# Kernel tuning notes

Hardware: AMD Instinct MI355X
Metric: run time of the kernel (lower is better)

The kernel has to match this reference:

```python
import jax, jax.numpy as jnp
import numpy as np

T, CH, D, H, W, K = 2, 8, 4, 128, 128, 2048


def setup_inputs() -> dict:
    key = jax.random.key(0)
    k1, k2, k3, k4, k5 = jax.random.split(key, 5)
    image_real = jax.random.normal(k1, (T, D, H, W), dtype=jnp.float32)
    image_imag = jax.random.normal(k2, (T, D, H, W), dtype=jnp.float32)
    csm_real = jax.random.normal(k3, (T, CH, D, H, W), dtype=jnp.float32)
    csm_imag = jax.random.normal(k4, (T, CH, D, H, W), dtype=jnp.float32)
    # non-uniform k-space trajectory in radians/voxel, [-pi, pi)
    traj = jax.random.uniform(k5, (T, 2, K), dtype=jnp.float32,
                              minval=-np.pi, maxval=np.pi)
    return {"image_real": image_real, "image_imag": image_imag,
            "csm_real": csm_real, "csm_imag": csm_imag, "traj": traj}


def reference(image_real, image_imag, csm_real, csm_imag, traj):
    # Coil-sensitivity encode: t d h w, t ch d h w -> t ch d h w (broadcast mul)
    image = (image_real + 1j * image_imag).astype(jnp.complex64)
    csm = (csm_real + 1j * csm_imag).astype(jnp.complex64)
    multi = image[:, None] * csm                       # [t, ch, d, h, w]
    t, ch, d, h, w = multi.shape
    k = traj.shape[-1]
    # Type-2 NUFFT over (h, w): exact nonuniform DFT with centered pixel grid
    ys = (jnp.arange(h) - h // 2).astype(jnp.float32)  # [h]
    xs = (jnp.arange(w) - w // 2).astype(jnp.float32)  # [w]
    # phase[t, k, h, w] = ky*y + kx*x
    phase = (traj[:, 0, :, None, None] * ys[None, None, :, None]
             + traj[:, 1, :, None, None] * xs[None, None, None, :])
    E = jnp.exp(-1j * phase).astype(jnp.complex64).reshape(t, k, h * w)
    img_flat = multi.reshape(t, ch * d, h * w)         # [t, ch*d, h*w]
    ksp = jnp.einsum('tnp,tkp->tnk', img_flat, E)      # [t, ch*d, k]
    return ksp.reshape(t, ch, d, k)
```

## Files before the change

### kernel.cpp

```cpp
#include <hip/hip_runtime.h>
#include <math.h>

typedef __attribute__((ext_vector_type(8))) short bf16x8;
typedef __attribute__((ext_vector_type(4))) float f32x4;

#define NK   2048
#define KT   16
#define NTHR 256

#define MULTI_ELEMS (1 << 20)
#define PART_OFF    (4u << 20)

__device__ __forceinline__ unsigned short f2bf(float f) {
    union { float f; unsigned u; } v; v.f = f;
    const unsigned r = (v.u + 0x7fffu + ((v.u >> 16) & 1u)) >> 16;
    return (unsigned short)r;
}

__global__ __launch_bounds__(256)
void make_multi_bf16(const float* __restrict__ imr, const float* __restrict__ imi,
                     const float* __restrict__ csr, const float* __restrict__ csi,
                     unsigned short* __restrict__ mRb, unsigned short* __restrict__ mIb)
{
    const int gid = blockIdx.x * 256 + threadIdx.x;
    const int p   = gid * 4;
    const int x   = p & 127;
    const int y   = (p >> 7) & 127;
    const int n   = (p >> 14) & 31;
    const int t   = p >> 19;
    const int d   = n & 3;
    const int ch  = n >> 2;
    const int io  = ((t * 4 + d) * 128 + y) * 128 + x;
    const int co  = (((t * 8 + ch) * 4 + d) * 128 + y) * 128 + x;

    const float4 ar = *(const float4*)(imr + io);
    const float4 ai = *(const float4*)(imi + io);
    const float4 br = *(const float4*)(csr + co);
    const float4 bi = *(const float4*)(csi + co);

    ushort4 sr, si;
    sr.x = f2bf(ar.x*br.x - ai.x*bi.x);  si.x = f2bf(ar.x*bi.x + ai.x*br.x);
    sr.y = f2bf(ar.y*br.y - ai.y*bi.y);  si.y = f2bf(ar.y*bi.y + ai.y*br.y);
    sr.z = f2bf(ar.z*br.z - ai.z*bi.z);  si.z = f2bf(ar.z*bi.z + ai.z*br.z);
    sr.w = f2bf(ar.w*br.w - ai.w*bi.w);  si.w = f2bf(ar.w*bi.w + ai.w*br.w);
    *(ushort4*)(mRb + p) = sr;
    *(ushort4*)(mIb + p) = si;
}

__global__ __launch_bounds__(NTHR, 4)
void nufft_mfma11(const float* __restrict__ traj,
                  const unsigned short* __restrict__ mRb,
                  const unsigned short* __restrict__ mIb,
                  float* __restrict__ part)
{
    __shared__ __align__(16) unsigned char sm[16384 + 2 * 64 * 136 * 2];
    float2 (*eyT)[16] = reinterpret_cast<float2 (*)[16]>(sm);
    float2 (*exT)[16] = reinterpret_cast<float2 (*)[16]>(sm + 16384);
    unsigned short (*aLds)[64][136] =
        reinterpret_cast<unsigned short (*)[64][136]>(sm + 16384);
    float (*red)[1024] = reinterpret_cast<float (*)[1024]>(sm + 16384);

    const int b   = blockIdx.x;
    const int xcd = b & 7;
    const int t   = xcd >> 2;
    const int idx = (xcd & 3) * 128 + (b >> 3);
    const int kt  = idx >> 2;
    const int yq  = idx & 3;
    const int k0  = kt * KT;
    const int tid = threadIdx.x;

    for (int i = tid; i < 2 * 128 * KT; i += NTHR) {
        const int ax  = i >> 11;
        const int rem = i & 2047;
        const int c   = rem >> 4;
        const int kli = rem & 15;
        const float kv = traj[(t * 2 + ax) * NK + k0 + kli];
        float s, co;
        sincosf(-kv * (float)(c - 64), &s, &co);
        if (ax == 0) eyT[c][kli] = make_float2(co, s);
        else         exT[c][kli] = make_float2(co, s);
    }
    __syncthreads();

    const int wv = tid >> 6;
    const int l  = tid & 63;
    const int kl = l & 15;
    const int g  = l >> 4;
    const int xw = wv * 32 + g * 8;

    bf16x8 bEr, bEiN, bEi;
#pragma unroll
    for (int j = 0; j < 8; ++j) {
        const float2 ex = exT[xw + j][kl];
        bEr[j]  = (short)f2bf(ex.x);
        bEiN[j] = (short)f2bf(-ex.y);
        bEi[j]  = (short)(bEiN[j] ^ (short)0x8000);
    }
    __syncthreads();

    f32x4 cR0 = {0.f,0.f,0.f,0.f}, cI0 = {0.f,0.f,0.f,0.f};
    f32x4 cR1 = {0.f,0.f,0.f,0.f}, cI1 = {0.f,0.f,0.f,0.f};

    for (int pp = 0; pp < 16; ++pp) {
        const int y0 = yq * 32 + pp * 2;

#pragma unroll
        for (int q = 0; q < 4; ++q) {
            const int s  = (q * 256 + tid) * 8;
            const int nr = s >> 7;
            const int x  = s & 127;
            const int n  = nr & 31;
            const int yy = nr >> 5;
            const size_t go = (((size_t)(t * 32 + n)) << 14) + (y0 + yy) * 128 + x;
            *(bf16x8*)&aLds[0][nr][x] = *(const bf16x8*)(mRb + go);
            *(bf16x8*)&aLds[1][nr][x] = *(const bf16x8*)(mIb + go);
        }
        __syncthreads();

        {
            const bf16x8 aR0 = *(const bf16x8*)&aLds[0][kl][xw];
            const bf16x8 aI0 = *(const bf16x8*)&aLds[1][kl][xw];
            const bf16x8 aR1 = *(const bf16x8*)&aLds[0][kl + 16][xw];
            const bf16x8 aI1 = *(const bf16x8*)&aLds[1][kl + 16][xw];

            f32x4 rR0 = {0.f,0.f,0.f,0.f}, rI0 = {0.f,0.f,0.f,0.f};
            f32x4 rR1 = {0.f,0.f,0.f,0.f}, rI1 = {0.f,0.f,0.f,0.f};

            rR0 = __builtin_amdgcn_mfma_f32_16x16x32_bf16(aR0, bEr,  rR0, 0, 0, 0);
            rR0 = __builtin_amdgcn_mfma_f32_16x16x32_bf16(aI0, bEiN, rR0, 0, 0, 0);
            rI0 = __builtin_amdgcn_mfma_f32_16x16x32_bf16(aR0, bEi,  rI0, 0, 0, 0);
            rI0 = __builtin_amdgcn_mfma_f32_16x16x32_bf16(aI0, bEr,  rI0, 0, 0, 0);
            rR1 = __builtin_amdgcn_mfma_f32_16x16x32_bf16(aR1, bEr,  rR1, 0, 0, 0);
            rR1 = __builtin_amdgcn_mfma_f32_16x16x32_bf16(aI1, bEiN, rR1, 0, 0, 0);
            rI1 = __builtin_amdgcn_mfma_f32_16x16x32_bf16(aR1, bEi,  rI1, 0, 0, 0);
            rI1 = __builtin_amdgcn_mfma_f32_16x16x32_bf16(aI1, bEr,  rI1, 0, 0, 0);

            const float2 e = eyT[y0][kl];
#pragma unroll
            for (int r = 0; r < 4; ++r) {
                cR0[r] += e.x * rR0[r] - e.y * rI0[r];
                cI0[r] += e.x * rI0[r] + e.y * rR0[r];
                cR1[r] += e.x * rR1[r] - e.y * rI1[r];
                cI1[r] += e.x * rI1[r] + e.y * rR1[r];
            }
        }

        {
            const bf16x8 aR0 = *(const bf16x8*)&aLds[0][32 + kl][xw];
            const bf16x8 aI0 = *(const bf16x8*)&aLds[1][32 + kl][xw];
            const bf16x8 aR1 = *(const bf16x8*)&aLds[0][32 + kl + 16][xw];
            const bf16x8 aI1 = *(const bf16x8*)&aLds[1][32 + kl + 16][xw];

            f32x4 rR0 = {0.f,0.f,0.f,0.f}, rI0 = {0.f,0.f,0.f,0.f};
            f32x4 rR1 = {0.f,0.f,0.f,0.f}, rI1 = {0.f,0.f,0.f,0.f};

            rR0 = __builtin_amdgcn_mfma_f32_16x16x32_bf16(aR0, bEr,  rR0, 0, 0, 0);
            rR0 = __builtin_amdgcn_mfma_f32_16x16x32_bf16(aI0, bEiN, rR0, 0, 0, 0);
            rI0 = __builtin_amdgcn_mfma_f32_16x16x32_bf16(aR0, bEi,  rI0, 0, 0, 0);
            rI0 = __builtin_amdgcn_mfma_f32_16x16x32_bf16(aI0, bEr,  rI0, 0, 0, 0);
            rR1 = __builtin_amdgcn_mfma_f32_16x16x32_bf16(aR1, bEr,  rR1, 0, 0, 0);
            rR1 = __builtin_amdgcn_mfma_f32_16x16x32_bf16(aI1, bEiN, rR1, 0, 0, 0);
            rI1 = __builtin_amdgcn_mfma_f32_16x16x32_bf16(aR1, bEi,  rI1, 0, 0, 0);
            rI1 = __builtin_amdgcn_mfma_f32_16x16x32_bf16(aI1, bEr,  rI1, 0, 0, 0);

            const float2 e = eyT[y0 + 1][kl];
#pragma unroll
            for (int r = 0; r < 4; ++r) {
                cR0[r] += e.x * rR0[r] - e.y * rI0[r];
                cI0[r] += e.x * rI0[r] + e.y * rR0[r];
                cR1[r] += e.x * rR1[r] - e.y * rI1[r];
                cI1[r] += e.x * rI1[r] + e.y * rR1[r];
            }
        }
        __syncthreads();
    }

    const int slot = wv & 1;
    if (wv < 2) {
#pragma unroll
        for (int r = 0; r < 4; ++r) {
            const int nn  = g * 4 + r;
            const int i00 = (nn * 16 + kl) * 2;
            const int i10 = ((nn + 16) * 16 + kl) * 2;
            red[slot][i00]     = cR0[r];
            red[slot][i00 + 1] = cI0[r];
            red[slot][i10]     = cR1[r];
            red[slot][i10 + 1] = cI1[r];
        }
    }
    __syncthreads();
    if (wv >= 2) {
#pragma unroll
        for (int r = 0; r < 4; ++r) {
            const int nn  = g * 4 + r;
            const int i00 = (nn * 16 + kl) * 2;
            const int i10 = ((nn + 16) * 16 + kl) * 2;
            red[slot][i00]     += cR0[r];
            red[slot][i00 + 1] += cI0[r];
            red[slot][i10]     += cR1[r];
            red[slot][i10 + 1] += cI1[r];
        }
    }
    __syncthreads();

    {
        const int bp = ((t * 128 + kt) * 4 + yq) * 1024;
        for (int f = tid; f < 1024; f += NTHR)
            part[bp + f] = red[0][f] + red[1][f];
    }
}

__global__ __launch_bounds__(256)
void reduce_out(const float* __restrict__ part, float* __restrict__ out)
{
    const int gidx = blockIdx.x * 256 + threadIdx.x;
    const int t  = gidx >> 16;
    const int r1 = gidx & 65535;
    const int kt = r1 >> 9;
    const int r2 = r1 & 511;
    const int n  = r2 >> 4;
    const int kl = r2 & 15;

    const int base = ((t * 128 + kt) * 4) * 1024;
    const int fr   = (n * 16 + kl) * 2;
    float re = 0.f, im = 0.f;
#pragma unroll
    for (int yqi = 0; yqi < 4; ++yqi) {
        re += part[base + yqi * 1024 + fr];
        im += part[base + yqi * 1024 + fr + 1];
    }

    const int oi = (t * 32 + n) * 2048 + kt * KT + kl;
    out[oi]           = re;
    out[131072 + oi]  = im;
}

extern "C" void kernel_launch(void* const* d_in, const int* in_sizes, int n_in,
                              void* d_out, int out_size, void* d_ws, size_t ws_size,
                              hipStream_t stream) {
    const float* imr  = (const float*)d_in[0];
    const float* imi  = (const float*)d_in[1];
    const float* csr  = (const float*)d_in[2];
    const float* csi  = (const float*)d_in[3];
    const float* traj = (const float*)d_in[4];
    float* out = (float*)d_out;

    unsigned short* mRb = (unsigned short*)d_ws;
    unsigned short* mIb = mRb + MULTI_ELEMS;
    float* part = (float*)((char*)d_ws + PART_OFF);

    make_multi_bf16<<<dim3(1024), dim3(256), 0, stream>>>(imr, imi, csr, csi, mRb, mIb);
    nufft_mfma11<<<dim3(1024), dim3(NTHR), 0, stream>>>(traj, mRb, mIb, part);
    reduce_out<<<dim3(512), dim3(256), 0, stream>>>(part, out);
}
```

Measured before the change: 60.36 us.

## Process two 16-wide k-tiles per block to reuse staged image tiles

Each block now covers 32 k-samples instead of 16, computing two sets of MFMA products from the same LDS-staged image rows, and the grid is halved to 512 blocks. This halves global/LDS loads of the bf16 coil image per unit of work and halves the per-block sincos table setup relative to output. In exchange it doubles accumulator register use, lowers the occupancy hint to 2 blocks per SIMD set, and leaves fewer blocks to fill the GPU.

```diff
diff --git a/kernel.cpp b/kernel.cpp
--- a/kernel.cpp
+++ b/kernel.cpp
@@ -5,7 +5,6 @@
 typedef __attribute__((ext_vector_type(4))) float f32x4;
 
 #define NK   2048
-#define KT   16
 #define NTHR 256
 
 #define MULTI_ELEMS (1 << 20)
@@ -47,33 +46,33 @@
     *(ushort4*)(mIb + p) = si;
 }
 
-__global__ __launch_bounds__(NTHR, 4)
-void nufft_mfma11(const float* __restrict__ traj,
+__global__ __launch_bounds__(NTHR, 2)
+void nufft_mfma12(const float* __restrict__ traj,
                   const unsigned short* __restrict__ mRb,
                   const unsigned short* __restrict__ mIb,
                   float* __restrict__ part)
 {
-    __shared__ __align__(16) unsigned char sm[16384 + 2 * 64 * 136 * 2];
-    float2 (*eyT)[16] = reinterpret_cast<float2 (*)[16]>(sm);
-    float2 (*exT)[16] = reinterpret_cast<float2 (*)[16]>(sm + 16384);
+    __shared__ __align__(16) unsigned char sm[32768 + 2 * 64 * 136 * 2];
+    float2 (*eyT)[32] = reinterpret_cast<float2 (*)[32]>(sm);
+    float2 (*exT)[32] = reinterpret_cast<float2 (*)[32]>(sm + 32768);
     unsigned short (*aLds)[64][136] =
-        reinterpret_cast<unsigned short (*)[64][136]>(sm + 16384);
-    float (*red)[1024] = reinterpret_cast<float (*)[1024]>(sm + 16384);
+        reinterpret_cast<unsigned short (*)[64][136]>(sm + 32768);
+    float (*red)[2048] = reinterpret_cast<float (*)[2048]>(sm + 32768);
 
     const int b   = blockIdx.x;
     const int xcd = b & 7;
     const int t   = xcd >> 2;
-    const int idx = (xcd & 3) * 128 + (b >> 3);
-    const int kt  = idx >> 2;
+    const int idx = (xcd & 3) * 64 + (b >> 3);
+    const int ktp = idx >> 2;
     const int yq  = idx & 3;
-    const int k0  = kt * KT;
+    const int k0  = ktp * 32;
     const int tid = threadIdx.x;
 
-    for (int i = tid; i < 2 * 128 * KT; i += NTHR) {
-        const int ax  = i >> 11;
-        const int rem = i & 2047;
-        const int c   = rem >> 4;
-        const int kli = rem & 15;
+    for (int i = tid; i < 2 * 128 * 32; i += NTHR) {
+        const int ax  = i >> 12;
+        const int rem = i & 4095;
+        const int c   = rem >> 5;
+        const int kli = rem & 31;
         const float kv = traj[(t * 2 + ax) * NK + k0 + kli];
         float s, co;
         sincosf(-kv * (float)(c - 64), &s, &co);
@@ -88,18 +87,24 @@
     const int g  = l >> 4;
     const int xw = wv * 32 + g * 8;
 
-    bf16x8 bEr, bEiN, bEi;
+    bf16x8 bEr_a, bEiN_a, bEi_a, bEr_b, bEiN_b, bEi_b;
 #pragma unroll
     for (int j = 0; j < 8; ++j) {
-        const float2 ex = exT[xw + j][kl];
-        bEr[j]  = (short)f2bf(ex.x);
-        bEiN[j] = (short)f2bf(-ex.y);
-        bEi[j]  = (short)(bEiN[j] ^ (short)0x8000);
+        const float2 exa = exT[xw + j][kl];
+        bEr_a[j]  = (short)f2bf(exa.x);
+        bEiN_a[j] = (short)f2bf(-exa.y);
+        bEi_a[j]  = (short)(bEiN_a[j] ^ (short)0x8000);
+        const float2 exb = exT[xw + j][16 + kl];
+        bEr_b[j]  = (short)f2bf(exb.x);
+        bEiN_b[j] = (short)f2bf(-exb.y);
+        bEi_b[j]  = (short)(bEiN_b[j] ^ (short)0x8000);
     }
     __syncthreads();
 
-    f32x4 cR0 = {0.f,0.f,0.f,0.f}, cI0 = {0.f,0.f,0.f,0.f};
-    f32x4 cR1 = {0.f,0.f,0.f,0.f}, cI1 = {0.f,0.f,0.f,0.f};
+    f32x4 cR0a = {0.f,0.f,0.f,0.f}, cI0a = {0.f,0.f,0.f,0.f};
+    f32x4 cR1a = {0.f,0.f,0.f,0.f}, cI1a = {0.f,0.f,0.f,0.f};
+    f32x4 cR0b = {0.f,0.f,0.f,0.f}, cI0b = {0.f,0.f,0.f,0.f};
+    f32x4 cR1b = {0.f,0.f,0.f,0.f}, cI1b = {0.f,0.f,0.f,0.f};
 
     for (int pp = 0; pp < 16; ++pp) {
         const int y0 = yq * 32 + pp * 2;
@@ -125,23 +130,44 @@
 
             f32x4 rR0 = {0.f,0.f,0.f,0.f}, rI0 = {0.f,0.f,0.f,0.f};
             f32x4 rR1 = {0.f,0.f,0.f,0.f}, rI1 = {0.f,0.f,0.f,0.f};
-
-            rR0 = __builtin_amdgcn_mfma_f32_16x16x32_bf16(aR0, bEr,  rR0, 0, 0, 0);
-            rR0 = __builtin_amdgcn_mfma_f32_16x16x32_bf16(aI0, bEiN, rR0, 0, 0, 0);
-            rI0 = __builtin_amdgcn_mfma_f32_16x16x32_bf16(aR0, bEi,  rI0, 0, 0, 0);
-            rI0 = __builtin_amdgcn_mfma_f32_16x16x32_bf16(aI0, bEr,  rI0, 0, 0, 0);
-            rR1 = __builtin_amdgcn_mfma_f32_16x16x32_bf16(aR1, bEr,  rR1, 0, 0, 0);
-            rR1 = __builtin_amdgcn_mfma_f32_16x16x32_bf16(aI1, bEiN, rR1, 0, 0, 0);
-            rI1 = __builtin_amdgcn_mfma_f32_16x16x32_bf16(aR1, bEi,  rI1, 0, 0, 0);
-            rI1 = __builtin_amdgcn_mfma_f32_16x16x32_bf16(aI1, bEr,  rI1, 0, 0, 0);
-
-            const float2 e = eyT[y0][kl];
-#pragma unroll
-            for (int r = 0; r < 4; ++r) {
-                cR0[r] += e.x * rR0[r] - e.y * rI0[r];
-                cI0[r] += e.x * rI0[r] + e.y * rR0[r];
-                cR1[r] += e.x * rR1[r] - e.y * rI1[r];
-                cI1[r] += e.x * rI1[r] + e.y * rR1[r];
+            rR0 = __builtin_amdgcn_mfma_f32_16x16x32_bf16(aR0, bEr_a,  rR0, 0, 0, 0);
+            rR0 = __builtin_amdgcn_mfma_f32_16x16x32_bf16(aI0, bEiN_a, rR0, 0, 0, 0);
+            rI0 = __builtin_amdgcn_mfma_f32_16x16x32_bf16(aR0, bEi_a,  rI0, 0, 0, 0);
+            rI0 = __builtin_amdgcn_mfma_f32_16x16x32_bf16(aI0, bEr_a,  rI0, 0, 0, 0);
+            rR1 = __builtin_amdgcn_mfma_f32_16x16x32_bf16(aR1, bEr_a,  rR1, 0, 0, 0);
+            rR1 = __builtin_amdgcn_mfma_f32_16x16x32_bf16(aI1, bEiN_a, rR1, 0, 0, 0);
+            rI1 = __builtin_amdgcn_mfma_f32_16x16x32_bf16(aR1, bEi_a,  rI1, 0, 0, 0);
+            rI1 = __builtin_amdgcn_mfma_f32_16x16x32_bf16(aI1, bEr_a,  rI1, 0, 0, 0);
+            {
+                const float2 e = eyT[y0][kl];
+#pragma unroll
+                for (int r = 0; r < 4; ++r) {
+                    cR0a[r] += e.x * rR0[r] - e.y * rI0[r];
+                    cI0a[r] += e.x * rI0[r] + e.y * rR0[r];
+                    cR1a[r] += e.x * rR1[r] - e.y * rI1[r];
+                    cI1a[r] += e.x * rI1[r] + e.y * rR1[r];
+                }
+            }
+
+            f32x4 sR0 = {0.f,0.f,0.f,0.f}, sI0 = {0.f,0.f,0.f,0.f};
+            f32x4 sR1 = {0.f,0.f,0.f,0.f}, sI1 = {0.f,0.f,0.f,0.f};
+            sR0 = __builtin_amdgcn_mfma_f32_16x16x32_bf16(aR0, bEr_b,  sR0, 0, 0, 0);
+            sR0 = __builtin_amdgcn_mfma_f32_16x16x32_bf16(aI0, bEiN_b, sR0, 0, 0, 0);
+            sI0 = __builtin_amdgcn_mfma_f32_16x16x32_bf16(aR0, bEi_b,  sI0, 0, 0, 0);
+            sI0 = __builtin_amdgcn_mfma_f32_16x16x32_bf16(aI0, bEr_b,  sI0, 0, 0, 0);
+            sR1 = __builtin_amdgcn_mfma_f32_16x16x32_bf16(aR1, bEr_b,  sR1, 0, 0, 0);
+            sR1 = __builtin_amdgcn_mfma_f32_16x16x32_bf16(aI1, bEiN_b, sR1, 0, 0, 0);
+            sI1 = __builtin_amdgcn_mfma_f32_16x16x32_bf16(aR1, bEi_b,  sI1, 0, 0, 0);
+            sI1 = __builtin_amdgcn_mfma_f32_16x16x32_bf16(aI1, bEr_b,  sI1, 0, 0, 0);
+            {
+                const float2 e = eyT[y0][16 + kl];
+#pragma unroll
+                for (int r = 0; r < 4; ++r) {
+                    cR0b[r] += e.x * sR0[r] - e.y * sI0[r];
+                    cI0b[r] += e.x * sI0[r] + e.y * sR0[r];
+                    cR1b[r] += e.x * sR1[r] - e.y * sI1[r];
+                    cI1b[r] += e.x * sI1[r] + e.y * sR1[r];
+                }
             }
         }
 
@@ -153,23 +179,44 @@
 
             f32x4 rR0 = {0.f,0.f,0.f,0.f}, rI0 = {0.f,0.f,0.f,0.f};
             f32x4 rR1 = {0.f,0.f,0.f,0.f}, rI1 = {0.f,0.f,0.f,0.f};
-
-            rR0 = __builtin_amdgcn_mfma_f32_16x16x32_bf16(aR0, bEr,  rR0, 0, 0, 0);
-            rR0 = __builtin_amdgcn_mfma_f32_16x16x32_bf16(aI0, bEiN, rR0, 0, 0, 0);
-            rI0 = __builtin_amdgcn_mfma_f32_16x16x32_bf16(aR0, bEi,  rI0, 0, 0, 0);
-            rI0 = __builtin_amdgcn_mfma_f32_16x16x32_bf16(aI0, bEr,  rI0, 0, 0, 0);
-            rR1 = __builtin_amdgcn_mfma_f32_16x16x32_bf16(aR1, bEr,  rR1, 0, 0, 0);
-            rR1 = __builtin_amdgcn_mfma_f32_16x16x32_bf16(aI1, bEiN, rR1, 0, 0, 0);
-            rI1 = __builtin_amdgcn_mfma_f32_16x16x32_bf16(aR1, bEi,  rI1, 0, 0, 0);
-            rI1 = __builtin_amdgcn_mfma_f32_16x16x32_bf16(aI1, bEr,  rI1, 0, 0, 0);
-
-            const float2 e = eyT[y0 + 1][kl];
-#pragma unroll
-            for (int r = 0; r < 4; ++r) {
-                cR0[r] += e.x * rR0[r] - e.y * rI0[r];
-                cI0[r] += e.x * rI0[r] + e.y * rR0[r];
-                cR1[r] += e.x * rR1[r] - e.y * rI1[r];
-                cI1[r] += e.x * rI1[r] + e.y * rR1[r];
+            rR0 = __builtin_amdgcn_mfma_f32_16x16x32_bf16(aR0, bEr_a,  rR0, 0, 0, 0);
+            rR0 = __builtin_amdgcn_mfma_f32_16x16x32_bf16(aI0, bEiN_a, rR0, 0, 0, 0);
+            rI0 = __builtin_amdgcn_mfma_f32_16x16x32_bf16(aR0, bEi_a,  rI0, 0, 0, 0);
+            rI0 = __builtin_amdgcn_mfma_f32_16x16x32_bf16(aI0, bEr_a,  rI0, 0, 0, 0);
+            rR1 = __builtin_amdgcn_mfma_f32_16x16x32_bf16(aR1, bEr_a,  rR1, 0, 0, 0);
+            rR1 = __builtin_amdgcn_mfma_f32_16x16x32_bf16(aI1, bEiN_a, rR1, 0, 0, 0);
+            rI1 = __builtin_amdgcn_mfma_f32_16x16x32_bf16(aR1, bEi_a,  rI1, 0, 0, 0);
+            rI1 = __builtin_amdgcn_mfma_f32_16x16x32_bf16(aI1, bEr_a,  rI1, 0, 0, 0);
+            {
+                const float2 e = eyT[y0 + 1][kl];
+#pragma unroll
+                for (int r = 0; r < 4; ++r) {
+                    cR0a[r] += e.x * rR0[r] - e.y * rI0[r];
+                    cI0a[r] += e.x * rI0[r] + e.y * rR0[r];
+                    cR1a[r] += e.x * rR1[r] - e.y * rI1[r];
+                    cI1a[r] += e.x * rI1[r] + e.y * rR1[r];
+                }
+            }
+
+            f32x4 sR0 = {0.f,0.f,0.f,0.f}, sI0 = {0.f,0.f,0.f,0.f};
+            f32x4 sR1 = {0.f,0.f,0.f,0.f}, sI1 = {0.f,0.f,0.f,0.f};
+            sR0 = __builtin_amdgcn_mfma_f32_16x16x32_bf16(aR0, bEr_b,  sR0, 0, 0, 0);
+            sR0 = __builtin_amdgcn_mfma_f32_16x16x32_bf16(aI0, bEiN_b, sR0, 0, 0, 0);
+            sI0 = __builtin_amdgcn_mfma_f32_16x16x32_bf16(aR0, bEi_b,  sI0, 0, 0, 0);
+            sI0 = __builtin_amdgcn_mfma_f32_16x16x32_bf16(aI0, bEr_b,  sI0, 0, 0, 0);
+            sR1 = __builtin_amdgcn_mfma_f32_16x16x32_bf16(aR1, bEr_b,  sR1, 0, 0, 0);
+            sR1 = __builtin_amdgcn_mfma_f32_16x16x32_bf16(aI1, bEiN_b, sR1, 0, 0, 0);
+            sI1 = __builtin_amdgcn_mfma_f32_16x16x32_bf16(aR1, bEi_b,  sI1, 0, 0, 0);
+            sI1 = __builtin_amdgcn_mfma_f32_16x16x32_bf16(aI1, bEr_b,  sI1, 0, 0, 0);
+            {
+                const float2 e = eyT[y0 + 1][16 + kl];
+#pragma unroll
+                for (int r = 0; r < 4; ++r) {
+                    cR0b[r] += e.x * sR0[r] - e.y * sI0[r];
+                    cI0b[r] += e.x * sI0[r] + e.y * sR0[r];
+                    cR1b[r] += e.x * sR1[r] - e.y * sI1[r];
+                    cI1b[r] += e.x * sI1[r] + e.y * sR1[r];
+                }
             }
         }
         __syncthreads();
@@ -182,10 +229,14 @@
             const int nn  = g * 4 + r;
             const int i00 = (nn * 16 + kl) * 2;
             const int i10 = ((nn + 16) * 16 + kl) * 2;
-            red[slot][i00]     = cR0[r];
-            red[slot][i00 + 1] = cI0[r];
-            red[slot][i10]     = cR1[r];
-            red[slot][i10 + 1] = cI1[r];
+            red[slot][i00]            = cR0a[r];
+            red[slot][i00 + 1]        = cI0a[r];
+            red[slot][i10]            = cR1a[r];
+            red[slot][i10 + 1]        = cI1a[r];
+            red[slot][1024 + i00]     = cR0b[r];
+            red[slot][1024 + i00 + 1] = cI0b[r];
+            red[slot][1024 + i10]     = cR1b[r];
+            red[slot][1024 + i10 + 1] = cI1b[r];
         }
     }
     __syncthreads();
@@ -195,17 +246,21 @@
             const int nn  = g * 4 + r;
             const int i00 = (nn * 16 + kl) * 2;
             const int i10 = ((nn + 16) * 16 + kl) * 2;
-            red[slot][i00]     += cR0[r];
-            red[slot][i00 + 1] += cI0[r];
-            red[slot][i10]     += cR1[r];
-            red[slot][i10 + 1] += cI1[r];
+            red[slot][i00]            += cR0a[r];
+            red[slot][i00 + 1]        += cI0a[r];
+            red[slot][i10]            += cR1a[r];
+            red[slot][i10 + 1]        += cI1a[r];
+            red[slot][1024 + i00]     += cR0b[r];
+            red[slot][1024 + i00 + 1] += cI0b[r];
+            red[slot][1024 + i10]     += cR1b[r];
+            red[slot][1024 + i10 + 1] += cI1b[r];
         }
     }
     __syncthreads();
 
     {
-        const int bp = ((t * 128 + kt) * 4 + yq) * 1024;
-        for (int f = tid; f < 1024; f += NTHR)
+        const int bp = ((t * 64 + ktp) * 4 + yq) * 2048;
+        for (int f = tid; f < 2048; f += NTHR)
             part[bp + f] = red[0][f] + red[1][f];
     }
 }
@@ -214,23 +269,26 @@
 void reduce_out(const float* __restrict__ part, float* __restrict__ out)
 {
     const int gidx = blockIdx.x * 256 + threadIdx.x;
-    const int t  = gidx >> 16;
-    const int r1 = gidx & 65535;
-    const int kt = r1 >> 9;
-    const int r2 = r1 & 511;
-    const int n  = r2 >> 4;
-    const int kl = r2 & 15;
-
-    const int base = ((t * 128 + kt) * 4) * 1024;
-    const int fr   = (n * 16 + kl) * 2;
+    const int t   = gidx >> 16;
+    const int r1  = gidx & 65535;
+    const int ktp = r1 >> 10;
+    const int r2  = r1 & 1023;
+    const int kg  = r2 >> 9;
+    const int r3  = r2 & 511;
+    const int n   = r3 >> 4;
+    const int kl  = r3 & 15;
+
+    const int base = ((t * 64 + ktp) * 4) * 2048;
+    const int fr   = kg * 1024 + (n * 16 + kl) * 2;
     float re = 0.f, im = 0.f;
 #pragma unroll
     for (int yqi = 0; yqi < 4; ++yqi) {
-        re += part[base + yqi * 1024 + fr];
-        im += part[base + yqi * 1024 + fr + 1];
-    }
-
-    const int oi = (t * 32 + n) * 2048 + kt * KT + kl;
+        re += part[base + yqi * 2048 + fr];
+        im += part[base + yqi * 2048 + fr + 1];
+    }
+
+    const int k  = ktp * 32 + kg * 16 + kl;
+    const int oi = (t * 32 + n) * 2048 + k;
     out[oi]           = re;
     out[131072 + oi]  = im;
 }
@@ -250,6 +308,6 @@
     float* part = (float*)((char*)d_ws + PART_OFF);
 
     make_multi_bf16<<<dim3(1024), dim3(256), 0, stream>>>(imr, imi, csr, csi, mRb, mIb);
-    nufft_mfma11<<<dim3(1024), dim3(NTHR), 0, stream>>>(traj, mRb, mIb, part);
+    nufft_mfma12<<<dim3(512), dim3(NTHR), 0, stream>>>(traj, mRb, mIb, part);
     reduce_out<<<dim3(512), dim3(256), 0, stream>>>(part, out);
 }
```

Result: faster. 48.41 us (median of 2 runs) (-19.8%).
